# Kernel tuning notes

Hardware: AMD Instinct MI355X
Metric: run time of the kernel (lower is better)

The kernel has to match this reference:

```python
import jax, jax.numpy as jnp
import numpy as np


def _gnn_layer(feat, W, b, src, dst, n_nodes):
    # edge-wise: gather src feats -> Linear -> scatter-sum at dst
    m = feat @ W + b                                   # [N, out]
    agg = jax.ops.segment_sum(m[src], dst, num_segments=n_nodes)  # [N, out]
    # concat aggregated messages with self-transformed features -> 2*out
    return jnp.concatenate([agg, m], axis=-1)


def setup_inputs() -> dict:
    key = jax.random.key(0)
    ks = jax.random.split(key, 6)
    N, E, D_IN, D_OUT = 50000, 800000, 128, 128
    features = jax.random.normal(ks[0], (N, D_IN), dtype=jnp.float32)
    src = jax.random.randint(ks[1], (E,), 0, N, dtype=jnp.int32)
    dst = jax.random.randint(ks[2], (E,), 0, N, dtype=jnp.int32)
    W1 = jax.random.normal(ks[3], (D_IN, D_OUT), dtype=jnp.float32) / np.sqrt(D_IN)
    b1 = jnp.zeros((D_OUT,), dtype=jnp.float32)
    W2 = jax.random.normal(ks[4], (2 * D_OUT, D_OUT), dtype=jnp.float32) / np.sqrt(2 * D_OUT)
    b2 = jnp.zeros((D_OUT,), dtype=jnp.float32)
    return {"features": features, "src": src, "dst": dst,
            "W1": W1, "b1": b1, "W2": W2, "b2": b2}


def reference(features, src, dst, W1, b1, W2, b2):
    n_nodes = features.shape[0]
    feat = _gnn_layer(features, W1, b1, src, dst, n_nodes)  # [N, 2*out]
    feat = _gnn_layer(feat, W2, b2, src, dst, n_nodes)      # [N, 2*out]
    return feat
```

## Files before the change

### kernel.cpp

```cpp
#include <hip/hip_runtime.h>


#define D 128
#define CBLK 256
#define DCAP 8192

typedef __attribute__((ext_vector_type(8))) short short8;
typedef __attribute__((ext_vector_type(4))) float float4v;
typedef unsigned short ushort_t;
typedef unsigned int uint_t;

static __device__ __forceinline__ ushort_t f2bf(float f) {
    uint_t u = __builtin_bit_cast(uint_t, f);
    u += 0x7FFFu + ((u >> 16) & 1u);
    return (ushort_t)(u >> 16);
}
static __device__ __forceinline__ float bfhi(uint_t u) {
    return __builtin_bit_cast(float, u & 0xFFFF0000u);
}
static __device__ __forceinline__ float bflo(uint_t u) {
    return __builtin_bit_cast(float, u << 16);
}

__global__ __launch_bounds__(256) void packw_binA(
    const float* __restrict__ W1, const float* __restrict__ W2,
    ushort_t* __restrict__ W1p, ushort_t* __restrict__ W2p,
    const int* __restrict__ dst, int* __restrict__ mat, int E, int NB)
{
    __shared__ int h[256];
    if (blockIdx.x < CBLK) {
        const int c = blockIdx.x;
        for (int i = threadIdx.x; i < NB; i += 256) h[i] = 0;
        __syncthreads();
        const int chunk = (E + CBLK - 1) / CBLK;
        int e0 = c * chunk, e1 = e0 + chunk; if (e1 > E) e1 = E;
        for (int e = e0 + threadIdx.x; e < e1; e += 256)
            atomicAdd(&h[dst[e] >> 8], 1);
        __syncthreads();
        for (int i = threadIdx.x; i < NB; i += 256)
            mat[i * CBLK + c] = h[i];
        return;
    }
    const int n1 = 4 * 8 * 64;
    const int n2 = 8 * 8 * 64;
    int t = (blockIdx.x - CBLK) * 256 + threadIdx.x;
    if (t >= n1 + n2) return;
    const float* W; ushort_t* Wp; int tt;
    if (t < n1) { W = W1; Wp = W1p; tt = t; }
    else        { W = W2; Wp = W2p; tt = t - n1; }
    int lane = tt & 63, cg = (tt >> 6) & 7, kb = tt >> 9;
    int krow = kb * 32 + (lane >> 4) * 8;
    int col  = cg * 16 + (lane & 15);
    #pragma unroll
    for (int j = 0; j < 8; ++j)
        Wp[(size_t)tt * 8 + j] = f2bf(W[(size_t)(krow + j) * D + col]);
}

__global__ __launch_bounds__(256) void binB(
    const int* __restrict__ mat, int* __restrict__ matc,
    int* __restrict__ bb, int* __restrict__ offs, int E, int N, int NB)
{
    __shared__ int s[256];
    __shared__ int ex[256];
    const int b = blockIdx.x;
    const int tid = threadIdx.x;

    int v = 0;
    if (tid < NB) {
        const int* row = &mat[tid * CBLK];
        for (int c = 0; c < CBLK; ++c) v += row[c];
    }
    s[tid] = v; __syncthreads();
    for (int o = 1; o < 256; o <<= 1) {
        int t = (tid >= o) ? s[tid - o] : 0;
        __syncthreads();
        s[tid] += t;
        __syncthreads();
    }
    ex[tid] = s[tid] - v;
    __syncthreads();
    if (b == 0) {
        if (tid < NB) bb[tid] = ex[tid];
        if (tid == 0) { bb[NB] = E; offs[N] = E; }
    }
    const int bbb = ex[b];

    int v2 = mat[b * CBLK + tid];
    __syncthreads();
    s[tid] = v2; __syncthreads();
    for (int o = 1; o < 256; o <<= 1) {
        int t = (tid >= o) ? s[tid - o] : 0;
        __syncthreads();
        s[tid] += t;
        __syncthreads();
    }
    matc[b * CBLK + tid] = bbb + s[tid] - v2;
}

__global__ __launch_bounds__(256) void binC_gemm1(
    const int* __restrict__ src, const int* __restrict__ dst,
    const int* __restrict__ matc, int2* __restrict__ tmp, int E, int NB,
    const float* __restrict__ X, const ushort_t* __restrict__ Wp,
    const float* __restrict__ bias, ushort_t* __restrict__ Ybf, int N)
{
    __shared__ int base[256];
    __shared__ int lcnt[256];
    if (blockIdx.x < CBLK) {
        const int c = blockIdx.x;
        for (int i = threadIdx.x; i < NB; i += 256) {
            base[i] = matc[i * CBLK + c];
            lcnt[i] = 0;
        }
        __syncthreads();
        const int chunk = (E + CBLK - 1) / CBLK;
        int e0 = c * chunk, e1 = e0 + chunk; if (e1 > E) e1 = E;
        for (int e = e0 + threadIdx.x; e < e1; e += 256) {
            int d = dst[e];
            int b = d >> 8;
            int p = base[b] + atomicAdd(&lcnt[b], 1);
            int2 pr; pr.x = d; pr.y = src[e];
            tmp[p] = pr;
        }
        return;
    }

    const int wave = threadIdx.x >> 6;
    const int lane = threadIdx.x & 63;
    const int quad = lane >> 4;
    const int l16  = lane & 15;
    const int r0   = (blockIdx.x - CBLK) * 128 + wave * 32;

    float4v acc[2][8];
    #pragma unroll
    for (int cg = 0; cg < 8; ++cg) {
        float bv = bias[cg * 16 + l16];
        float4v b4 = {bv, bv, bv, bv};
        acc[0][cg] = b4; acc[1][cg] = b4;
    }

    const short8* wp8 = (const short8*)Wp;

    #pragma unroll
    for (int kb = 0; kb < 4; ++kb) {
        const int k0 = kb * 32 + quad * 8;
        short8 a[2];
        #pragma unroll
        for (int rb = 0; rb < 2; ++rb) {
            int row = r0 + rb * 16 + l16;
            if (row >= N) row = N - 1;
            const float* p = &X[(size_t)row * D + k0];
            float4 x0 = *(const float4*)p;
            float4 x1 = *(const float4*)(p + 4);
            short8 s;
            s[0] = (short)f2bf(x0.x); s[1] = (short)f2bf(x0.y);
            s[2] = (short)f2bf(x0.z); s[3] = (short)f2bf(x0.w);
            s[4] = (short)f2bf(x1.x); s[5] = (short)f2bf(x1.y);
            s[6] = (short)f2bf(x1.z); s[7] = (short)f2bf(x1.w);
            a[rb] = s;
        }
        #pragma unroll
        for (int cg = 0; cg < 8; ++cg) {
            short8 b = wp8[(kb * 8 + cg) * 64 + lane];
            acc[0][cg] = __builtin_amdgcn_mfma_f32_16x16x32_bf16(a[0], b, acc[0][cg], 0, 0, 0);
            acc[1][cg] = __builtin_amdgcn_mfma_f32_16x16x32_bf16(a[1], b, acc[1][cg], 0, 0, 0);
        }
    }

    #pragma unroll
    for (int rb = 0; rb < 2; ++rb) {
        int rowb = r0 + rb * 16 + quad * 4;
        #pragma unroll
        for (int cg = 0; cg < 8; ++cg) {
            int col = cg * 16 + l16;
            #pragma unroll
            for (int i = 0; i < 4; ++i) {
                int row = rowb + i;
                if (row < N) Ybf[(size_t)row * D + col] = f2bf(acc[rb][cg][i]);
            }
        }
    }
}

__global__ __launch_bounds__(256) void binD(const int2* __restrict__ tmp,
                                            const int* __restrict__ bb,
                                            int* __restrict__ offs,
                                            int* __restrict__ bsrc, int N, int NB) {
    __shared__ int hist[256];
    __shared__ int foff[256];
    __shared__ int cntf[256];
    __shared__ int outS[DCAP];
    const int b = blockIdx.x;
    const int tid = threadIdx.x;
    const int beg = bb[b], end = bb[b + 1];
    const int cnt = end - beg;
    const int n0 = b << 8;

    hist[tid] = 0;
    __syncthreads();
    for (int i = tid; i < cnt; i += 256)
        atomicAdd(&hist[tmp[beg + i].x & 255], 1);
    __syncthreads();
    int v = hist[tid];
    __syncthreads();
    hist[tid] = v; __syncthreads();
    for (int o = 1; o < 256; o <<= 1) {
        int t = (tid >= o) ? hist[tid - o] : 0;
        __syncthreads();
        hist[tid] += t;
        __syncthreads();
    }
    foff[tid] = hist[tid] - v;
    cntf[tid] = 0;
    __syncthreads();

    int node = n0 + tid;
    if (node < N) offs[node] = beg + foff[tid];

    if (cnt <= DCAP) {
        for (int i = tid; i < cnt; i += 256) {
            int2 p = tmp[beg + i];
            int f = p.x & 255;
            int pos = foff[f] + atomicAdd(&cntf[f], 1);
            outS[pos] = p.y;
        }
        __syncthreads();
        for (int i = tid; i < cnt; i += 256)
            bsrc[beg + i] = outS[i];
    } else {
        for (int i = tid; i < cnt; i += 256) {
            int2 p = tmp[beg + i];
            int f = p.x & 255;
            int pos = foff[f] + atomicAdd(&cntf[f], 1);
            bsrc[beg + pos] = p.y;
        }
    }
}

__global__ __launch_bounds__(256) void gemm2_mfma(
    const ushort_t* __restrict__ A0, const ushort_t* __restrict__ A1,
    const ushort_t* __restrict__ Wp, const float* __restrict__ bias,
    float* __restrict__ Yf, ushort_t* __restrict__ Ybf, int N)
{
    const int wave = threadIdx.x >> 6;
    const int lane = threadIdx.x & 63;
    const int quad = lane >> 4;
    const int l16  = lane & 15;
    const int r0   = blockIdx.x * 128 + wave * 32;

    float4v acc[2][8];
    #pragma unroll
    for (int cg = 0; cg < 8; ++cg) {
        float bv = bias[cg * 16 + l16];
        float4v b4 = {bv, bv, bv, bv};
        acc[0][cg] = b4; acc[1][cg] = b4;
    }

    const short8* wp8 = (const short8*)Wp;

    #pragma unroll
    for (int kb = 0; kb < 8; ++kb) {
        const ushort_t* __restrict__ A = (kb < 4) ? A0 : A1;
        const int k0 = (kb & 3) * 32 + quad * 8;
        short8 a[2];
        #pragma unroll
        for (int rb = 0; rb < 2; ++rb) {
            int row = r0 + rb * 16 + l16;
            if (row >= N) row = N - 1;
            a[rb] = *(const short8*)&A[(size_t)row * D + k0];
        }
        #pragma unroll
        for (int cg = 0; cg < 8; ++cg) {
            short8 b = wp8[(kb * 8 + cg) * 64 + lane];
            acc[0][cg] = __builtin_amdgcn_mfma_f32_16x16x32_bf16(a[0], b, acc[0][cg], 0, 0, 0);
            acc[1][cg] = __builtin_amdgcn_mfma_f32_16x16x32_bf16(a[1], b, acc[1][cg], 0, 0, 0);
        }
    }

    #pragma unroll
    for (int rb = 0; rb < 2; ++rb) {
        int rowb = r0 + rb * 16 + quad * 4;
        #pragma unroll
        for (int cg = 0; cg < 8; ++cg) {
            int col = cg * 16 + l16;
            #pragma unroll
            for (int i = 0; i < 4; ++i) {
                int row = rowb + i;
                if (row < N) {
                    float v = acc[rb][cg][i];
                    Yf[(size_t)row * 256 + col] = v;
                    Ybf[(size_t)row * D + col] = f2bf(v);
                }
            }
        }
    }
}

__global__ __launch_bounds__(256) void gather_bf(
    const ushort_t* __restrict__ msg,
    const int* __restrict__ offs, const int* __restrict__ bsrc,
    ushort_t* __restrict__ aggB,
    float* __restrict__ aggF,
    int N)
{
    int node = (blockIdx.x * 256 + threadIdx.x) >> 6;
    int lane = threadIdx.x & 63;
    if (node >= N) return;
    const int quad = lane >> 4;
    const int c16  = lane & 15;
    int beg = offs[node], end = offs[node + 1];

    float ax[4] = {0.f, 0.f, 0.f, 0.f};
    float ay[4] = {0.f, 0.f, 0.f, 0.f};
    const uint4* mp = (const uint4*)msg;

    for (int base = beg; base < end; base += 64) {
        int cnt = end - base; if (cnt > 64) cnt = 64;
        int sidx = bsrc[base + (lane < cnt ? lane : cnt - 1)];
        for (int j0 = 0; j0 < cnt; j0 += 16) {
            #pragma unroll
            for (int t = 0; t < 4; ++t) {
                int e  = j0 + t * 4 + quad;
                int ec = (e < cnt) ? e : cnt - 1;
                int s  = __shfl(sidx, ec, 64);
                uint4 u = mp[(size_t)s * 16 + c16];
                if (e < cnt) {
                    ax[0] += bflo(u.x); ay[0] += bfhi(u.x);
                    ax[1] += bflo(u.y); ay[1] += bfhi(u.y);
                    ax[2] += bflo(u.z); ay[2] += bfhi(u.z);
                    ax[3] += bflo(u.w); ay[3] += bfhi(u.w);
                }
            }
        }
    }

    #pragma unroll
    for (int k = 0; k < 4; ++k) {
        ax[k] += __shfl_xor(ax[k], 16, 64);
        ax[k] += __shfl_xor(ax[k], 32, 64);
        ay[k] += __shfl_xor(ay[k], 16, 64);
        ay[k] += __shfl_xor(ay[k], 32, 64);
    }

    if (quad == 0) {
        if (aggB) {
            uint4 o;
            o.x = (uint_t)f2bf(ax[0]) | ((uint_t)f2bf(ay[0]) << 16);
            o.y = (uint_t)f2bf(ax[1]) | ((uint_t)f2bf(ay[1]) << 16);
            o.z = (uint_t)f2bf(ax[2]) | ((uint_t)f2bf(ay[2]) << 16);
            o.w = (uint_t)f2bf(ax[3]) | ((uint_t)f2bf(ay[3]) << 16);
            ((uint4*)aggB)[(size_t)node * 16 + c16] = o;
        } else {
            float4 w0 = {ax[0], ay[0], ax[1], ay[1]};
            float4 w1 = {ax[2], ay[2], ax[3], ay[3]};
            float* p = &aggF[(size_t)node * 256 + c16 * 8];
            *(float4*)p = w0;
            *(float4*)(p + 4) = w1;
        }
    }
}

extern "C" void kernel_launch(void* const* d_in, const int* in_sizes, int n_in,
                              void* d_out, int out_size, void* d_ws, size_t ws_size,
                              hipStream_t stream) {
    const float* features = (const float*)d_in[0];
    const int*   src      = (const int*)d_in[1];
    const int*   dst      = (const int*)d_in[2];
    const float* W1       = (const float*)d_in[3];
    const float* b1       = (const float*)d_in[4];
    const float* W2       = (const float*)d_in[5];
    const float* b2       = (const float*)d_in[6];
    float* out = (float*)d_out;

    const int N = in_sizes[0] / D;
    const int E = in_sizes[1];
    const int NB = (N + 255) >> 8;

    ushort_t* m1bf   = (ushort_t*)d_ws;
    ushort_t* agg1bf = m1bf + (size_t)N * D;
    ushort_t* m2bf   = agg1bf + (size_t)N * D;
    ushort_t* W1p    = m2bf + (size_t)N * D;
    ushort_t* W2p    = W1p + 16384;
    int*  mat  = (int*)(W2p + 32768);
    int*  matc = mat + (size_t)NB * CBLK;
    int*  bb   = matc + (size_t)NB * CBLK;
    int*  offs = bb + NB + 1;
    int2* tmp  = (int2*)(offs + N + 1);
    int*  bsrc = (int*)(tmp + (size_t)E);

    const int gemmBlocks = (N + 127) / 128;

    packw_binA<<<CBLK + 24, 256, 0, stream>>>(W1, W2, W1p, W2p, dst, mat, E, NB);
    binB<<<NB, 256, 0, stream>>>(mat, matc, bb, offs, E, N, NB);
    binC_gemm1<<<CBLK + gemmBlocks, 256, 0, stream>>>(src, dst, matc, tmp, E, NB,
                                                      features, W1p, b1, m1bf, N);
    binD<<<NB, 256, 0, stream>>>(tmp, bb, offs, bsrc, N, NB);
    gather_bf<<<(N * 64 + 255) / 256, 256, 0, stream>>>(m1bf, offs, bsrc,
                                                        agg1bf, nullptr, N);
    gemm2_mfma<<<gemmBlocks, 256, 0, stream>>>(agg1bf, m1bf, W2p, b2,
                                               out + D, m2bf, N);
    gather_bf<<<(N * 64 + 255) / 256, 256, 0, stream>>>(m2bf, offs, bsrc,
                                                        nullptr, out, N);
}
```

Measured before the change: 208.5 us.

## Split gemm1 across binning kernels and chunk gather by column groups

Pulls the first GEMM body into a shared device function and divides its row blocks between the binC scatter kernel and the binD per-node sort kernel, so that GEMM work overlaps both binning phases. The gather kernel is rewritten so each wave handles one node and one quarter of the feature columns, with the four chunks spread over separate blocks; each 16-lane group handles its own edge, replacing the shuffle-broadcast loop. DCAP is reduced to lower LDS use in binD, which raises occupancy now that it also runs GEMM blocks, at the risk of overflowing for high-degree buckets. The chunked gather re-reads offsets and source indices four times per node.

```diff
diff --git a/kernel.cpp b/kernel.cpp
--- a/kernel.cpp
+++ b/kernel.cpp
@@ -3,7 +3,7 @@
 
 #define D 128
 #define CBLK 256
-#define DCAP 8192
+#define DCAP 6144
 
 typedef __attribute__((ext_vector_type(8))) short short8;
 typedef __attribute__((ext_vector_type(4))) float float4v;
@@ -22,113 +22,16 @@
     return __builtin_bit_cast(float, u << 16);
 }
 
-__global__ __launch_bounds__(256) void packw_binA(
-    const float* __restrict__ W1, const float* __restrict__ W2,
-    ushort_t* __restrict__ W1p, ushort_t* __restrict__ W2p,
-    const int* __restrict__ dst, int* __restrict__ mat, int E, int NB)
-{
-    __shared__ int h[256];
-    if (blockIdx.x < CBLK) {
-        const int c = blockIdx.x;
-        for (int i = threadIdx.x; i < NB; i += 256) h[i] = 0;
-        __syncthreads();
-        const int chunk = (E + CBLK - 1) / CBLK;
-        int e0 = c * chunk, e1 = e0 + chunk; if (e1 > E) e1 = E;
-        for (int e = e0 + threadIdx.x; e < e1; e += 256)
-            atomicAdd(&h[dst[e] >> 8], 1);
-        __syncthreads();
-        for (int i = threadIdx.x; i < NB; i += 256)
-            mat[i * CBLK + c] = h[i];
-        return;
-    }
-    const int n1 = 4 * 8 * 64;
-    const int n2 = 8 * 8 * 64;
-    int t = (blockIdx.x - CBLK) * 256 + threadIdx.x;
-    if (t >= n1 + n2) return;
-    const float* W; ushort_t* Wp; int tt;
-    if (t < n1) { W = W1; Wp = W1p; tt = t; }
-    else        { W = W2; Wp = W2p; tt = t - n1; }
-    int lane = tt & 63, cg = (tt >> 6) & 7, kb = tt >> 9;
-    int krow = kb * 32 + (lane >> 4) * 8;
-    int col  = cg * 16 + (lane & 15);
-    #pragma unroll
-    for (int j = 0; j < 8; ++j)
-        Wp[(size_t)tt * 8 + j] = f2bf(W[(size_t)(krow + j) * D + col]);
-}
-
-__global__ __launch_bounds__(256) void binB(
-    const int* __restrict__ mat, int* __restrict__ matc,
-    int* __restrict__ bb, int* __restrict__ offs, int E, int N, int NB)
-{
-    __shared__ int s[256];
-    __shared__ int ex[256];
-    const int b = blockIdx.x;
-    const int tid = threadIdx.x;
-
-    int v = 0;
-    if (tid < NB) {
-        const int* row = &mat[tid * CBLK];
-        for (int c = 0; c < CBLK; ++c) v += row[c];
-    }
-    s[tid] = v; __syncthreads();
-    for (int o = 1; o < 256; o <<= 1) {
-        int t = (tid >= o) ? s[tid - o] : 0;
-        __syncthreads();
-        s[tid] += t;
-        __syncthreads();
-    }
-    ex[tid] = s[tid] - v;
-    __syncthreads();
-    if (b == 0) {
-        if (tid < NB) bb[tid] = ex[tid];
-        if (tid == 0) { bb[NB] = E; offs[N] = E; }
-    }
-    const int bbb = ex[b];
-
-    int v2 = mat[b * CBLK + tid];
-    __syncthreads();
-    s[tid] = v2; __syncthreads();
-    for (int o = 1; o < 256; o <<= 1) {
-        int t = (tid >= o) ? s[tid - o] : 0;
-        __syncthreads();
-        s[tid] += t;
-        __syncthreads();
-    }
-    matc[b * CBLK + tid] = bbb + s[tid] - v2;
-}
-
-__global__ __launch_bounds__(256) void binC_gemm1(
-    const int* __restrict__ src, const int* __restrict__ dst,
-    const int* __restrict__ matc, int2* __restrict__ tmp, int E, int NB,
+static __device__ __forceinline__ void gemm1_body(
     const float* __restrict__ X, const ushort_t* __restrict__ Wp,
-    const float* __restrict__ bias, ushort_t* __restrict__ Ybf, int N)
-{
-    __shared__ int base[256];
-    __shared__ int lcnt[256];
-    if (blockIdx.x < CBLK) {
-        const int c = blockIdx.x;
-        for (int i = threadIdx.x; i < NB; i += 256) {
-            base[i] = matc[i * CBLK + c];
-            lcnt[i] = 0;
-        }
-        __syncthreads();
-        const int chunk = (E + CBLK - 1) / CBLK;
-        int e0 = c * chunk, e1 = e0 + chunk; if (e1 > E) e1 = E;
-        for (int e = e0 + threadIdx.x; e < e1; e += 256) {
-            int d = dst[e];
-            int b = d >> 8;
-            int p = base[b] + atomicAdd(&lcnt[b], 1);
-            int2 pr; pr.x = d; pr.y = src[e];
-            tmp[p] = pr;
-        }
-        return;
-    }
-
+    const float* __restrict__ bias, ushort_t* __restrict__ Ybf,
+    int N, int gb)
+{
     const int wave = threadIdx.x >> 6;
     const int lane = threadIdx.x & 63;
     const int quad = lane >> 4;
     const int l16  = lane & 15;
-    const int r0   = (blockIdx.x - CBLK) * 128 + wave * 32;
+    const int r0   = gb * 128 + wave * 32;
 
     float4v acc[2][8];
     #pragma unroll
@@ -181,14 +84,124 @@
     }
 }
 
-__global__ __launch_bounds__(256) void binD(const int2* __restrict__ tmp,
-                                            const int* __restrict__ bb,
-                                            int* __restrict__ offs,
-                                            int* __restrict__ bsrc, int N, int NB) {
+__global__ __launch_bounds__(256) void packw_binA(
+    const float* __restrict__ W1, const float* __restrict__ W2,
+    ushort_t* __restrict__ W1p, ushort_t* __restrict__ W2p,
+    const int* __restrict__ dst, int* __restrict__ mat, int E, int NB)
+{
+    __shared__ int h[256];
+    if (blockIdx.x < CBLK) {
+        const int c = blockIdx.x;
+        for (int i = threadIdx.x; i < NB; i += 256) h[i] = 0;
+        __syncthreads();
+        const int chunk = (E + CBLK - 1) / CBLK;
+        int e0 = c * chunk, e1 = e0 + chunk; if (e1 > E) e1 = E;
+        for (int e = e0 + threadIdx.x; e < e1; e += 256)
+            atomicAdd(&h[dst[e] >> 8], 1);
+        __syncthreads();
+        for (int i = threadIdx.x; i < NB; i += 256)
+            mat[i * CBLK + c] = h[i];
+        return;
+    }
+    const int n1 = 4 * 8 * 64;
+    const int n2 = 8 * 8 * 64;
+    int t = (blockIdx.x - CBLK) * 256 + threadIdx.x;
+    if (t >= n1 + n2) return;
+    const float* W; ushort_t* Wp; int tt;
+    if (t < n1) { W = W1; Wp = W1p; tt = t; }
+    else        { W = W2; Wp = W2p; tt = t - n1; }
+    int lane = tt & 63, cg = (tt >> 6) & 7, kb = tt >> 9;
+    int krow = kb * 32 + (lane >> 4) * 8;
+    int col  = cg * 16 + (lane & 15);
+    #pragma unroll
+    for (int j = 0; j < 8; ++j)
+        Wp[(size_t)tt * 8 + j] = f2bf(W[(size_t)(krow + j) * D + col]);
+}
+
+__global__ __launch_bounds__(256) void binB(
+    const int* __restrict__ mat, int* __restrict__ matc,
+    int* __restrict__ bb, int* __restrict__ offs, int E, int N, int NB)
+{
+    __shared__ int s[256];
+    __shared__ int ex[256];
+    const int b = blockIdx.x;
+    const int tid = threadIdx.x;
+
+    int v = 0;
+    if (tid < NB) {
+        const int* row = &mat[tid * CBLK];
+        for (int c = 0; c < CBLK; ++c) v += row[c];
+    }
+    s[tid] = v; __syncthreads();
+    for (int o = 1; o < 256; o <<= 1) {
+        int t = (tid >= o) ? s[tid - o] : 0;
+        __syncthreads();
+        s[tid] += t;
+        __syncthreads();
+    }
+    ex[tid] = s[tid] - v;
+    __syncthreads();
+    if (b == 0) {
+        if (tid < NB) bb[tid] = ex[tid];
+        if (tid == 0) { bb[NB] = E; offs[N] = E; }
+    }
+    const int bbb = ex[b];
+
+    int v2 = mat[b * CBLK + tid];
+    __syncthreads();
+    s[tid] = v2; __syncthreads();
+    for (int o = 1; o < 256; o <<= 1) {
+        int t = (tid >= o) ? s[tid - o] : 0;
+        __syncthreads();
+        s[tid] += t;
+        __syncthreads();
+    }
+    matc[b * CBLK + tid] = bbb + s[tid] - v2;
+}
+
+__global__ __launch_bounds__(256) void binC_gemm1(
+    const int* __restrict__ src, const int* __restrict__ dst,
+    const int* __restrict__ matc, int2* __restrict__ tmp, int E, int NB,
+    const float* __restrict__ X, const ushort_t* __restrict__ Wp,
+    const float* __restrict__ bias, ushort_t* __restrict__ Ybf, int N)
+{
+    __shared__ int base[256];
+    __shared__ int lcnt[256];
+    if (blockIdx.x < CBLK) {
+        const int c = blockIdx.x;
+        for (int i = threadIdx.x; i < NB; i += 256) {
+            base[i] = matc[i * CBLK + c];
+            lcnt[i] = 0;
+        }
+        __syncthreads();
+        const int chunk = (E + CBLK - 1) / CBLK;
+        int e0 = c * chunk, e1 = e0 + chunk; if (e1 > E) e1 = E;
+        for (int e = e0 + threadIdx.x; e < e1; e += 256) {
+            int d = dst[e];
+            int b = d >> 8;
+            int p = base[b] + atomicAdd(&lcnt[b], 1);
+            int2 pr; pr.x = d; pr.y = src[e];
+            tmp[p] = pr;
+        }
+        return;
+    }
+    gemm1_body(X, Wp, bias, Ybf, N, blockIdx.x - CBLK);
+}
+
+__global__ __launch_bounds__(256) void binD_gemm1(
+    const int2* __restrict__ tmp, const int* __restrict__ bb,
+    int* __restrict__ offs, int* __restrict__ bsrc, int N, int NB,
+    const float* __restrict__ X, const ushort_t* __restrict__ Wp,
+    const float* __restrict__ bias, ushort_t* __restrict__ Ybf, int gb0)
+{
     __shared__ int hist[256];
     __shared__ int foff[256];
     __shared__ int cntf[256];
     __shared__ int outS[DCAP];
+    if (blockIdx.x >= (uint_t)NB) {
+        gemm1_body(X, Wp, bias, Ybf, N, blockIdx.x - NB + gb0);
+        return;
+    }
     const int b = blockIdx.x;
     const int tid = threadIdx.x;
     const int beg = bb[b], end = bb[b + 1];
@@ -295,64 +308,61 @@
     }
 }
 
-__global__ __launch_bounds__(256) void gather_bf(
+__global__ __launch_bounds__(256) void gather_chunk(
     const ushort_t* __restrict__ msg,
     const int* __restrict__ offs, const int* __restrict__ bsrc,
     ushort_t* __restrict__ aggB,
     float* __restrict__ aggF,
-    int N)
-{
-    int node = (blockIdx.x * 256 + threadIdx.x) >> 6;
-    int lane = threadIdx.x & 63;
+    int N, int nodeBlks)
+{
+    const int chunk = blockIdx.x / nodeBlks;
+    const int nb    = blockIdx.x - chunk * nodeBlks;
+    const int wave  = threadIdx.x >> 6;
+    const int node  = nb * 4 + wave;
     if (node >= N) return;
-    const int quad = lane >> 4;
-    const int c16  = lane & 15;
-    int beg = offs[node], end = offs[node + 1];
+    const int lane = threadIdx.x & 63;
+    const int e4   = lane & 15;
+    const int g4   = chunk * 4 + (lane >> 4);
+
+    const int beg = offs[node], end = offs[node + 1];
 
     float ax[4] = {0.f, 0.f, 0.f, 0.f};
     float ay[4] = {0.f, 0.f, 0.f, 0.f};
     const uint4* mp = (const uint4*)msg;
 
-    for (int base = beg; base < end; base += 64) {
-        int cnt = end - base; if (cnt > 64) cnt = 64;
-        int sidx = bsrc[base + (lane < cnt ? lane : cnt - 1)];
-        for (int j0 = 0; j0 < cnt; j0 += 16) {
-            #pragma unroll
-            for (int t = 0; t < 4; ++t) {
-                int e  = j0 + t * 4 + quad;
-                int ec = (e < cnt) ? e : cnt - 1;
-                int s  = __shfl(sidx, ec, 64);
-                uint4 u = mp[(size_t)s * 16 + c16];
-                if (e < cnt) {
-                    ax[0] += bflo(u.x); ay[0] += bfhi(u.x);
-                    ax[1] += bflo(u.y); ay[1] += bfhi(u.y);
-                    ax[2] += bflo(u.z); ay[2] += bfhi(u.z);
-                    ax[3] += bflo(u.w); ay[3] += bfhi(u.w);
-                }
-            }
+    for (int base = beg; base < end; base += 16) {
+        int cnt = end - base; if (cnt > 16) cnt = 16;
+        if (e4 < cnt) {
+            int s = bsrc[base + e4];
+            uint4 u = mp[(size_t)s * 16 + g4];
+            ax[0] += bflo(u.x); ay[0] += bfhi(u.x);
+            ax[1] += bflo(u.y); ay[1] += bfhi(u.y);
+            ax[2] += bflo(u.z); ay[2] += bfhi(u.z);
+            ax[3] += bflo(u.w); ay[3] += bfhi(u.w);
         }
     }
 
     #pragma unroll
     for (int k = 0; k < 4; ++k) {
-        ax[k] += __shfl_xor(ax[k], 16, 64);
-        ax[k] += __shfl_xor(ax[k], 32, 64);
-        ay[k] += __shfl_xor(ay[k], 16, 64);
-        ay[k] += __shfl_xor(ay[k], 32, 64);
-    }
-
-    if (quad == 0) {
+        #pragma unroll
+        for (int m = 1; m <= 8; m <<= 1) {
+            ax[k] += __shfl_xor(ax[k], m, 64);
+            ay[k] += __shfl_xor(ay[k], m, 64);
+        }
+    }
+
+    if (e4 == 0) {
         if (aggB) {
             uint4 o;
             o.x = (uint_t)f2bf(ax[0]) | ((uint_t)f2bf(ay[0]) << 16);
             o.y = (uint_t)f2bf(ax[1]) | ((uint_t)f2bf(ay[1]) << 16);
             o.z = (uint_t)f2bf(ax[2]) | ((uint_t)f2bf(ay[2]) << 16);
             o.w = (uint_t)f2bf(ax[3]) | ((uint_t)f2bf(ay[3]) << 16);
-            ((uint4*)aggB)[(size_t)node * 16 + c16] = o;
+            ((uint4*)aggB)[(size_t)node * 16 + g4] = o;
         } else {
             float4 w0 = {ax[0], ay[0], ax[1], ay[1]};
             float4 w1 = {ax[2], ay[2], ax[3], ay[3]};
-            float* p = &aggF[(size_t)node * 256 + c16 * 8];
+            float* p = &aggF[(size_t)node * 256 + g4 * 8];
             *(float4*)p = w0;
             *(float4*)(p + 4) = w1;
         }
@@ -388,16 +398,19 @@
     int*  bsrc = (int*)(tmp + (size_t)E);
 
     const int gemmBlocks = (N + 127) / 128;
+    const int gbA = (gemmBlocks * 3) / 5;
+    const int nodeBlks = (N + 3) / 4;
 
     packw_binA<<<CBLK + 24, 256, 0, stream>>>(W1, W2, W1p, W2p, dst, mat, E, NB);
     binB<<<NB, 256, 0, stream>>>(mat, matc, bb, offs, E, N, NB);
-    binC_gemm1<<<CBLK + gemmBlocks, 256, 0, stream>>>(src, dst, matc, tmp, E, NB,
-                                                      features, W1p, b1, m1bf, N);
-    binD<<<NB, 256, 0, stream>>>(tmp, bb, offs, bsrc, N, NB);
-    gather_bf<<<(N * 64 + 255) / 256, 256, 0, stream>>>(m1bf, offs, bsrc,
-                                                        agg1bf, nullptr, N);
+    binC_gemm1<<<CBLK + gbA, 256, 0, stream>>>(src, dst, matc, tmp, E, NB,
+                                               features, W1p, b1, m1bf, N);
+    binD_gemm1<<<NB + (gemmBlocks - gbA), 256, 0, stream>>>(
+        tmp, bb, offs, bsrc, N, NB, features, W1p, b1, m1bf, gbA);
+    gather_chunk<<<nodeBlks * 4, 256, 0, stream>>>(m1bf, offs, bsrc,
+                                                   agg1bf, nullptr, N, nodeBlks);
     gemm2_mfma<<<gemmBlocks, 256, 0, stream>>>(agg1bf, m1bf, W2p, b2,
                                                out + D, m2bf, N);
-    gather_bf<<<(N * 64 + 255) / 256, 256, 0, stream>>>(m2bf, offs, bsrc,
-                                                        nullptr, out, N);
-}
+    gather_chunk<<<nodeBlks * 4, 256, 0, stream>>>(m2bf, offs, bsrc,
+                                                   nullptr, out, N, nodeBlks);
+}
```

New measurement: 291.1 us. 1.4x slower.

## Replace two-level bucket sort CSR build with global atomic degree histogram

Applied to the files above, without the earlier changes.

Swaps the blocked two-pass counting sort (per-chunk bucket histograms, bucket scan, bucket scatter into a temp pair buffer, then a per-bucket local sort) for a direct CSR build. The new path zeroes a per-node degree array, counts with global atomics, scans to get offsets, and scatters src ids through a per-node atomic cursor. This drops the intermediate int2 buffer pass and the binD kernel, at the cost of heavy global atomic traffic on 50K counters. Edge order within each node's list is now nondeterministic, so the fp summation order in the gathers changes from run to run.

```diff
diff --git a/kernel.cpp b/kernel.cpp
--- a/kernel.cpp
+++ b/kernel.cpp
@@ -2,8 +2,7 @@
 
 
 #define D 128
-#define CBLK 256
-#define DCAP 8192
+#define SCB 256
 
 typedef __attribute__((ext_vector_type(8))) short short8;
 typedef __attribute__((ext_vector_type(4))) float float4v;
@@ -22,113 +21,16 @@
     return __builtin_bit_cast(float, u << 16);
 }
 
-__global__ __launch_bounds__(256) void packw_binA(
-    const float* __restrict__ W1, const float* __restrict__ W2,
-    ushort_t* __restrict__ W1p, ushort_t* __restrict__ W2p,
-    const int* __restrict__ dst, int* __restrict__ mat, int E, int NB)
-{
-    __shared__ int h[256];
-    if (blockIdx.x < CBLK) {
-        const int c = blockIdx.x;
-        for (int i = threadIdx.x; i < NB; i += 256) h[i] = 0;
-        __syncthreads();
-        const int chunk = (E + CBLK - 1) / CBLK;
-        int e0 = c * chunk, e1 = e0 + chunk; if (e1 > E) e1 = E;
-        for (int e = e0 + threadIdx.x; e < e1; e += 256)
-            atomicAdd(&h[dst[e] >> 8], 1);
-        __syncthreads();
-        for (int i = threadIdx.x; i < NB; i += 256)
-            mat[i * CBLK + c] = h[i];
-        return;
-    }
-    const int n1 = 4 * 8 * 64;
-    const int n2 = 8 * 8 * 64;
-    int t = (blockIdx.x - CBLK) * 256 + threadIdx.x;
-    if (t >= n1 + n2) return;
-    const float* W; ushort_t* Wp; int tt;
-    if (t < n1) { W = W1; Wp = W1p; tt = t; }
-    else        { W = W2; Wp = W2p; tt = t - n1; }
-    int lane = tt & 63, cg = (tt >> 6) & 7, kb = tt >> 9;
-    int krow = kb * 32 + (lane >> 4) * 8;
-    int col  = cg * 16 + (lane & 15);
-    #pragma unroll
-    for (int j = 0; j < 8; ++j)
-        Wp[(size_t)tt * 8 + j] = f2bf(W[(size_t)(krow + j) * D + col]);
-}
-
-__global__ __launch_bounds__(256) void binB(
-    const int* __restrict__ mat, int* __restrict__ matc,
-    int* __restrict__ bb, int* __restrict__ offs, int E, int N, int NB)
-{
-    __shared__ int s[256];
-    __shared__ int ex[256];
-    const int b = blockIdx.x;
-    const int tid = threadIdx.x;
-
-    int v = 0;
-    if (tid < NB) {
-        const int* row = &mat[tid * CBLK];
-        for (int c = 0; c < CBLK; ++c) v += row[c];
-    }
-    s[tid] = v; __syncthreads();
-    for (int o = 1; o < 256; o <<= 1) {
-        int t = (tid >= o) ? s[tid - o] : 0;
-        __syncthreads();
-        s[tid] += t;
-        __syncthreads();
-    }
-    ex[tid] = s[tid] - v;
-    __syncthreads();
-    if (b == 0) {
-        if (tid < NB) bb[tid] = ex[tid];
-        if (tid == 0) { bb[NB] = E; offs[N] = E; }
-    }
-    const int bbb = ex[b];
-
-    int v2 = mat[b * CBLK + tid];
-    __syncthreads();
-    s[tid] = v2; __syncthreads();
-    for (int o = 1; o < 256; o <<= 1) {
-        int t = (tid >= o) ? s[tid - o] : 0;
-        __syncthreads();
-        s[tid] += t;
-        __syncthreads();
-    }
-    matc[b * CBLK + tid] = bbb + s[tid] - v2;
-}
-
-__global__ __launch_bounds__(256) void binC_gemm1(
-    const int* __restrict__ src, const int* __restrict__ dst,
-    const int* __restrict__ matc, int2* __restrict__ tmp, int E, int NB,
+static __device__ __forceinline__ void gemm1_body(
     const float* __restrict__ X, const ushort_t* __restrict__ Wp,
-    const float* __restrict__ bias, ushort_t* __restrict__ Ybf, int N)
-{
-    __shared__ int base[256];
-    __shared__ int lcnt[256];
-    if (blockIdx.x < CBLK) {
-        const int c = blockIdx.x;
-        for (int i = threadIdx.x; i < NB; i += 256) {
-            base[i] = matc[i * CBLK + c];
-            lcnt[i] = 0;
-        }
-        __syncthreads();
-        const int chunk = (E + CBLK - 1) / CBLK;
-        int e0 = c * chunk, e1 = e0 + chunk; if (e1 > E) e1 = E;
-        for (int e = e0 + threadIdx.x; e < e1; e += 256) {
-            int d = dst[e];
-            int b = d >> 8;
-            int p = base[b] + atomicAdd(&lcnt[b], 1);
-            int2 pr; pr.x = d; pr.y = src[e];
-            tmp[p] = pr;
-        }
-        return;
-    }
-
+    const float* __restrict__ bias, ushort_t* __restrict__ Ybf,
+    int N, int gb)
+{
     const int wave = threadIdx.x >> 6;
     const int lane = threadIdx.x & 63;
     const int quad = lane >> 4;
     const int l16  = lane & 15;
-    const int r0   = (blockIdx.x - CBLK) * 128 + wave * 32;
+    const int r0   = gb * 128 + wave * 32;
 
     float4v acc[2][8];
     #pragma unroll
@@ -181,59 +83,94 @@
     }
 }
 
-__global__ __launch_bounds__(256) void binD(const int2* __restrict__ tmp,
-                                            const int* __restrict__ bb,
-                                            int* __restrict__ offs,
-                                            int* __restrict__ bsrc, int N, int NB) {
-    __shared__ int hist[256];
-    __shared__ int foff[256];
-    __shared__ int cntf[256];
-    __shared__ int outS[DCAP];
+__global__ __launch_bounds__(256) void zero_pack(
+    const float* __restrict__ W1, const float* __restrict__ W2,
+    ushort_t* __restrict__ W1p, ushort_t* __restrict__ W2p,
+    int* __restrict__ deg, int ZB)
+{
+    if ((int)blockIdx.x < ZB) {
+        deg[blockIdx.x * 256 + threadIdx.x] = 0;
+        return;
+    }
+    const int n1 = 4 * 8 * 64;
+    const int n2 = 8 * 8 * 64;
+    int t = (blockIdx.x - ZB) * 256 + threadIdx.x;
+    if (t >= n1 + n2) return;
+    const float* W; ushort_t* Wp; int tt;
+    if (t < n1) { W = W1; Wp = W1p; tt = t; }
+    else        { W = W2; Wp = W2p; tt = t - n1; }
+    int lane = tt & 63, cg = (tt >> 6) & 7, kb = tt >> 9;
+    int krow = kb * 32 + (lane >> 4) * 8;
+    int col  = cg * 16 + (lane & 15);
+    #pragma unroll
+    for (int j = 0; j < 8; ++j)
+        Wp[(size_t)tt * 8 + j] = f2bf(W[(size_t)(krow + j) * D + col]);
+}
+
+__global__ __launch_bounds__(256) void hist(const int* __restrict__ dst,
+                                            int* __restrict__ deg, int E)
+{
+    int t = blockIdx.x * 256 + threadIdx.x;
+    for (int e = t; e < E; e += 256 * 256)
+        atomicAdd(&deg[dst[e]], 1);
+}
+
+__global__ __launch_bounds__(256) void scanK(
+    const int* __restrict__ deg, int* __restrict__ offs, int* __restrict__ cur,
+    int E, int N, int NB)
+{
+    __shared__ int s[256];
+    __shared__ int ex[256];
     const int b = blockIdx.x;
     const int tid = threadIdx.x;
-    const int beg = bb[b], end = bb[b + 1];
-    const int cnt = end - beg;
-    const int n0 = b << 8;
-
-    hist[tid] = 0;
+
+    int v = 0;
+    if (tid < NB) {
+        const int* p = &deg[tid * 256];
+        for (int i = 0; i < 256; ++i) v += p[i];
+    }
+    s[tid] = v; __syncthreads();
+    for (int o = 1; o < 256; o <<= 1) {
+        int t = (tid >= o) ? s[tid - o] : 0;
+        __syncthreads();
+        s[tid] += t;
+        __syncthreads();
+    }
+    ex[tid] = s[tid] - v;
     __syncthreads();
-    for (int i = tid; i < cnt; i += 256)
-        atomicAdd(&hist[tmp[beg + i].x & 255], 1);
+    const int cbase = ex[b];
+
+    int node = b * 256 + tid;
+    int d = deg[node];
     __syncthreads();
-    int v = hist[tid];
-    __syncthreads();
-    hist[tid] = v; __syncthreads();
+    s[tid] = d; __syncthreads();
     for (int o = 1; o < 256; o <<= 1) {
-        int t = (tid >= o) ? hist[tid - o] : 0;
+        int t = (tid >= o) ? s[tid - o] : 0;
         __syncthreads();
-        hist[tid] += t;
+        s[tid] += t;
         __syncthreads();
     }
-    foff[tid] = hist[tid] - v;
-    cntf[tid] = 0;
-    __syncthreads();
-
-    int node = n0 + tid;
-    if (node < N) offs[node] = beg + foff[tid];
-
-    if (cnt <= DCAP) {
-        for (int i = tid; i < cnt; i += 256) {
-            int2 p = tmp[beg + i];
-            int f = p.x & 255;
-            int pos = foff[f] + atomicAdd(&cntf[f], 1);
-            outS[pos] = p.y;
-        }
-        __syncthreads();
-        for (int i = tid; i < cnt; i += 256)
-            bsrc[beg + i] = outS[i];
-    } else {
-        for (int i = tid; i < cnt; i += 256) {
-            int2 p = tmp[beg + i];
-            int f = p.x & 255;
-            int pos = foff[f] + atomicAdd(&cntf[f], 1);
-            bsrc[beg + pos] = p.y;
-        }
-    }
+    int off = cbase + s[tid] - d;
+    if (node < N) { offs[node] = off; cur[node] = off; }
+    if (b == 0 && tid == 0) offs[N] = E;
+}
+
+__global__ __launch_bounds__(256) void scatter_gemm1(
+    const int* __restrict__ src, const int* __restrict__ dst,
+    int* __restrict__ cur, int* __restrict__ bsrc, int E,
+    const float* __restrict__ X, const ushort_t* __restrict__ Wp,
+    const float* __restrict__ bias, ushort_t* __restrict__ Ybf, int N)
+{
+    if ((int)blockIdx.x < SCB) {
+        int t = blockIdx.x * 256 + threadIdx.x;
+        for (int e = t; e < E; e += SCB * 256) {
+            int d = dst[e];
+            int pos = atomicAdd(&cur[d], 1);
+            bsrc[pos] = src[e];
+        }
+        return;
+    }
+    gemm1_body(X, Wp, bias, Ybf, N, blockIdx.x - SCB);
 }
 
 __global__ __launch_bounds__(256) void gemm2_mfma(
@@ -380,20 +317,20 @@
     ushort_t* m2bf   = agg1bf + (size_t)N * D;
     ushort_t* W1p    = m2bf + (size_t)N * D;
     ushort_t* W2p    = W1p + 16384;
-    int*  mat  = (int*)(W2p + 32768);
-    int*  matc = mat + (size_t)NB * CBLK;
-    int*  bb   = matc + (size_t)NB * CBLK;
+    int*  deg  = (int*)(W2p + 32768);
+    int*  cur  = deg + (size_t)NB * 256;
+    int*  bb   = cur + (size_t)NB * 256;
     int*  offs = bb + NB + 1;
     int2* tmp  = (int2*)(offs + N + 1);
     int*  bsrc = (int*)(tmp + (size_t)E);
 
     const int gemmBlocks = (N + 127) / 128;
 
-    packw_binA<<<CBLK + 24, 256, 0, stream>>>(W1, W2, W1p, W2p, dst, mat, E, NB);
-    binB<<<NB, 256, 0, stream>>>(mat, matc, bb, offs, E, N, NB);
-    binC_gemm1<<<CBLK + gemmBlocks, 256, 0, stream>>>(src, dst, matc, tmp, E, NB,
-                                                      features, W1p, b1, m1bf, N);
-    binD<<<NB, 256, 0, stream>>>(tmp, bb, offs, bsrc, N, NB);
+    zero_pack<<<NB + 24, 256, 0, stream>>>(W1, W2, W1p, W2p, deg, NB);
+    hist<<<256, 256, 0, stream>>>(dst, deg, E);
+    scanK<<<NB, 256, 0, stream>>>(deg, offs, cur, E, N, NB);
+    scatter_gemm1<<<SCB + gemmBlocks, 256, 0, stream>>>(
+        src, dst, cur, bsrc, E, features, W1p, b1, m1bf, N);
     gather_bf<<<(N * 64 + 255) / 256, 256, 0, stream>>>(m1bf, offs, bsrc,
                                                         agg1bf, nullptr, N);
     gemm2_mfma<<<gemmBlocks, 256, 0, stream>>>(agg1bf, m1bf, W2p, b2,
```

Measured after the change: 254.0 us. +21.8%, slower.

## Split gemm1 across binC and binD launches and halve GEMM tile rows

Applied to the files above, without the earlier changes.

The first GEMM is split so that about 3/5 of its row blocks run alongside binC and the rest run as extra blocks in the binD launch, filling idle CUs during the sort phases. Both GEMMs move from 128-row to 64-row blocks (16 rows per wave), which doubles the block count and lowers register pressure. The binD shared buffer capacity drops from 8192 to 6144 to improve occupancy, which risks overflowing if a bin holds more edges than fit.

```diff
diff --git a/kernel.cpp b/kernel.cpp
--- a/kernel.cpp
+++ b/kernel.cpp
@@ -3,7 +3,7 @@
 
 #define D 128
 #define CBLK 256
-#define DCAP 8192
+#define DCAP 6144
 
 typedef __attribute__((ext_vector_type(8))) short short8;
 typedef __attribute__((ext_vector_type(4))) float float4v;
@@ -20,6 +20,59 @@
 }
 static __device__ __forceinline__ float bflo(uint_t u) {
     return __builtin_bit_cast(float, u << 16);
+}
+
+static __device__ __forceinline__ void gemm1_body(
+    const float* __restrict__ X, const ushort_t* __restrict__ Wp,
+    const float* __restrict__ bias, ushort_t* __restrict__ Ybf,
+    int N, int gb)
+{
+    const int wave = threadIdx.x >> 6;
+    const int lane = threadIdx.x & 63;
+    const int quad = lane >> 4;
+    const int l16  = lane & 15;
+    const int r0   = gb * 64 + wave * 16;
+
+    float4v acc[8];
+    #pragma unroll
+    for (int cg = 0; cg < 8; ++cg) {
+        float bv = bias[cg * 16 + l16];
+        float4v b4 = {bv, bv, bv, bv};
+        acc[cg] = b4;
+    }
+
+    const short8* wp8 = (const short8*)Wp;
+
+    #pragma unroll
+    for (int kb = 0; kb < 4; ++kb) {
+        const int k0 = kb * 32 + quad * 8;
+        int row = r0 + l16;
+        if (row >= N) row = N - 1;
+        const float* p = &X[(size_t)row * D + k0];
+        float4 x0 = *(const float4*)p;
+        float4 x1 = *(const float4*)(p + 4);
+        short8 a;
+        a[0] = (short)f2bf(x0.x); a[1] = (short)f2bf(x0.y);
+        a[2] = (short)f2bf(x0.z); a[3] = (short)f2bf(x0.w);
+        a[4] = (short)f2bf(x1.x); a[5] = (short)f2bf(x1.y);
+        a[6] = (short)f2bf(x1.z); a[7] = (short)f2bf(x1.w);
+        #pragma unroll
+        for (int cg = 0; cg < 8; ++cg) {
+            short8 b = wp8[(kb * 8 + cg) * 64 + lane];
+            acc[cg] = __builtin_amdgcn_mfma_f32_16x16x32_bf16(a, b, acc[cg], 0, 0, 0);
+        }
+    }
+
+    const int rowb = r0 + quad * 4;
+    #pragma unroll
+    for (int cg = 0; cg < 8; ++cg) {
+        int col = cg * 16 + l16;
+        #pragma unroll
+        for (int i = 0; i < 4; ++i) {
+            int row = rowb + i;
+            if (row < N) Ybf[(size_t)row * D + col] = f2bf(acc[cg][i]);
+        }
+    }
 }
 
 __global__ __launch_bounds__(256) void packw_binA(
@@ -123,72 +176,23 @@
         }
         return;
     }
-
-    const int wave = threadIdx.x >> 6;
-    const int lane = threadIdx.x & 63;
-    const int quad = lane >> 4;
-    const int l16  = lane & 15;
-    const int r0   = (blockIdx.x - CBLK) * 128 + wave * 32;
-
-    float4v acc[2][8];
-    #pragma unroll
-    for (int cg = 0; cg < 8; ++cg) {
-        float bv = bias[cg * 16 + l16];
-        float4v b4 = {bv, bv, bv, bv};
-        acc[0][cg] = b4; acc[1][cg] = b4;
-    }
-
-    const short8* wp8 = (const short8*)Wp;
-
-    #pragma unroll
-    for (int kb = 0; kb < 4; ++kb) {
-        const int k0 = kb * 32 + quad * 8;
-        short8 a[2];
-        #pragma unroll
-        for (int rb = 0; rb < 2; ++rb) {
-            int row = r0 + rb * 16 + l16;
-            if (row >= N) row = N - 1;
-            const float* p = &X[(size_t)row * D + k0];
-            float4 x0 = *(const float4*)p;
-            float4 x1 = *(const float4*)(p + 4);
-            short8 s;
-            s[0] = (short)f2bf(x0.x); s[1] = (short)f2bf(x0.y);
-            s[2] = (short)f2bf(x0.z); s[3] = (short)f2bf(x0.w);
-            s[4] = (short)f2bf(x1.x); s[5] = (short)f2bf(x1.y);
-            s[6] = (short)f2bf(x1.z); s[7] = (short)f2bf(x1.w);
-            a[rb] = s;
-        }
-        #pragma unroll
-        for (int cg = 0; cg < 8; ++cg) {
-            short8 b = wp8[(kb * 8 + cg) * 64 + lane];
-            acc[0][cg] = __builtin_amdgcn_mfma_f32_16x16x32_bf16(a[0], b, acc[0][cg], 0, 0, 0);
-            acc[1][cg] = __builtin_amdgcn_mfma_f32_16x16x32_bf16(a[1], b, acc[1][cg], 0, 0, 0);
-        }
-    }
-
-    #pragma unroll
-    for (int rb = 0; rb < 2; ++rb) {
-        int rowb = r0 + rb * 16 + quad * 4;
-        #pragma unroll
-        for (int cg = 0; cg < 8; ++cg) {
-            int col = cg * 16 + l16;
-            #pragma unroll
-            for (int i = 0; i < 4; ++i) {
-                int row = rowb + i;
-                if (row < N) Ybf[(size_t)row * D + col] = f2bf(acc[rb][cg][i]);
-            }
-        }
-    }
-}
-
-__global__ __launch_bounds__(256) void binD(const int2* __restrict__ tmp,
-                                            const int* __restrict__ bb,
-                                            int* __restrict__ offs,
-                                            int* __restrict__ bsrc, int N, int NB) {
+    gemm1_body(X, Wp, bias, Ybf, N, blockIdx.x - CBLK);
+}
+
+__global__ __launch_bounds__(256) void binD_gemm1(
+    const int2* __restrict__ tmp, const int* __restrict__ bb,
+    int* __restrict__ offs, int* __restrict__ bsrc, int N, int NB,
+    const float* __restrict__ X, const ushort_t* __restrict__ Wp,
+    const float* __restrict__ bias, ushort_t* __restrict__ Ybf, int gb0)
+{
     __shared__ int hist[256];
     __shared__ int foff[256];
     __shared__ int cntf[256];
     __shared__ int outS[DCAP];
+    if (blockIdx.x >= (uint_t)NB) {
+        gemm1_body(X, Wp, bias, Ybf, N, blockIdx.x - NB + gb0);
+        return;
+    }
     const int b = blockIdx.x;
     const int tid = threadIdx.x;
     const int beg = bb[b], end = bb[b + 1];
@@ -245,14 +249,14 @@
     const int lane = threadIdx.x & 63;
     const int quad = lane >> 4;
     const int l16  = lane & 15;
-    const int r0   = blockIdx.x * 128 + wave * 32;
-
-    float4v acc[2][8];
+    const int r0   = blockIdx.x * 64 + wave * 16;
+
+    float4v acc[8];
     #pragma unroll
     for (int cg = 0; cg < 8; ++cg) {
         float bv = bias[cg * 16 + l16];
         float4v b4 = {bv, bv, bv, bv};
-        acc[0][cg] = b4; acc[1][cg] = b4;
+        acc[cg] = b4;
     }
 
     const short8* wp8 = (const short8*)Wp;
@@ -261,35 +265,27 @@
     for (int kb = 0; kb < 8; ++kb) {
         const ushort_t* __restrict__ A = (kb < 4) ? A0 : A1;
         const int k0 = (kb & 3) * 32 + quad * 8;
-        short8 a[2];
-        #pragma unroll
-        for (int rb = 0; rb < 2; ++rb) {
-            int row = r0 + rb * 16 + l16;
-            if (row >= N) row = N - 1;
-            a[rb] = *(const short8*)&A[(size_t)row * D + k0];
-        }
+        int row = r0 + l16;
+        if (row >= N) row = N - 1;
+        short8 a = *(const short8*)&A[(size_t)row * D + k0];
         #pragma unroll
         for (int cg = 0; cg < 8; ++cg) {
             short8 b = wp8[(kb * 8 + cg) * 64 + lane];
-            acc[0][cg] = __builtin_amdgcn_mfma_f32_16x16x32_bf16(a[0], b, acc[0][cg], 0, 0, 0);
-            acc[1][cg] = __builtin_amdgcn_mfma_f32_16x16x32_bf16(a[1], b, acc[1][cg], 0, 0, 0);
-        }
-    }
-
-    #pragma unroll
-    for (int rb = 0; rb < 2; ++rb) {
-        int rowb = r0 + rb * 16 + quad * 4;
+            acc[cg] = __builtin_amdgcn_mfma_f32_16x16x32_bf16(a, b, acc[cg], 0, 0, 0);
+        }
+    }
+
+    const int rowb = r0 + quad * 4;
+    #pragma unroll
+    for (int cg = 0; cg < 8; ++cg) {
+        int col = cg * 16 + l16;
         #pragma unroll
-        for (int cg = 0; cg < 8; ++cg) {
-            int col = cg * 16 + l16;
-            #pragma unroll
-            for (int i = 0; i < 4; ++i) {
-                int row = rowb + i;
-                if (row < N) {
-                    float v = acc[rb][cg][i];
-                    Yf[(size_t)row * 256 + col] = v;
-                    Ybf[(size_t)row * D + col] = f2bf(v);
-                }
+        for (int i = 0; i < 4; ++i) {
+            int row = rowb + i;
+            if (row < N) {
+                float v = acc[cg][i];
+                Yf[(size_t)row * 256 + col] = v;
+                Ybf[(size_t)row * D + col] = f2bf(v);
             }
         }
     }
@@ -387,13 +383,15 @@
     int2* tmp  = (int2*)(offs + N + 1);
     int*  bsrc = (int*)(tmp + (size_t)E);
 
-    const int gemmBlocks = (N + 127) / 128;
+    const int gemmBlocks = (N + 63) / 64;
+    const int gbA = (gemmBlocks * 3) / 5;
 
     packw_binA<<<CBLK + 24, 256, 0, stream>>>(W1, W2, W1p, W2p, dst, mat, E, NB);
     binB<<<NB, 256, 0, stream>>>(mat, matc, bb, offs, E, N, NB);
-    binC_gemm1<<<CBLK + gemmBlocks, 256, 0, stream>>>(src, dst, matc, tmp, E, NB,
-                                                      features, W1p, b1, m1bf, N);
-    binD<<<NB, 256, 0, stream>>>(tmp, bb, offs, bsrc, N, NB);
+    binC_gemm1<<<CBLK + gbA, 256, 0, stream>>>(src, dst, matc, tmp, E, NB,
+                                               features, W1p, b1, m1bf, N);
+    binD_gemm1<<<NB + (gemmBlocks - gbA), 256, 0, stream>>>(
+        tmp, bb, offs, bsrc, N, NB, features, W1p, b1, m1bf, gbA);
     gather_bf<<<(N * 64 + 255) / 256, 256, 0, stream>>>(m1bf, offs, bsrc,
                                                         agg1bf, nullptr, N);
     gemm2_mfma<<<gemmBlocks, 256, 0, stream>>>(agg1bf, m1bf, W2p, b2,
```

Result: no change. 205.5 us (-1.5%).
